# Kernel optimization log

Hardware: AMD Instinct MI355X
Metric: run time of the kernel (lower is better)

## Reference

```python
import jax, jax.numpy as jnp
import numpy as np

N_NODES = 100000
N_EDGES = 320000
DIM = 256


def _graph_conv(src, dst, h, W, b):
    # DGL GraphConv, norm='both', in_feats == out_feats (aggregate-then-transform)
    ones = jnp.ones((src.shape[0],), dtype=h.dtype)
    out_deg = jnp.clip(jax.ops.segment_sum(ones, src, num_segments=N_NODES), 1.0)
    in_deg = jnp.clip(jax.ops.segment_sum(ones, dst, num_segments=N_NODES), 1.0)
    h = h * (out_deg ** -0.5)[:, None]          # src-side normalization
    agg = jax.ops.segment_sum(h[src], dst, num_segments=N_NODES)  # SpMM (copy_u, sum)
    agg = agg * (in_deg ** -0.5)[:, None]       # dst-side normalization
    return agg @ W + b


def setup_inputs() -> dict:
    key = jax.random.key(0)
    ks = jax.random.split(key, 7)
    src = jax.random.randint(ks[0], (N_EDGES,), 0, N_NODES, dtype=jnp.int32)
    dst = jax.random.randint(ks[1], (N_EDGES,), 0, N_NODES, dtype=jnp.int32)
    node_feature = jax.random.normal(ks[2], (N_NODES, DIM), dtype=jnp.float32)
    s = 1.0 / np.sqrt(DIM)
    W1 = jax.random.normal(ks[3], (DIM, DIM), dtype=jnp.float32) * s
    b1 = jnp.zeros((DIM,), dtype=jnp.float32)
    W2 = jax.random.normal(ks[4], (DIM, DIM), dtype=jnp.float32) * s
    b2 = jnp.zeros((DIM,), dtype=jnp.float32)
    return {"src": src, "dst": dst, "node_feature": node_feature,
            "W1": W1, "b1": b1, "W2": W2, "b2": b2}


def reference(src, dst, node_feature, W1, b1, W2, b2):
    h = _graph_conv(src, dst, node_feature, W1, b1)
    h = _graph_conv(src, dst, jax.nn.relu(h), W2, b2)
    return jax.nn.relu(h)
```

## Files before the change

kernel.cpp:

```cpp
#include <hip/hip_runtime.h>

#define NN 100000
#define NE 320000
#define DIM 256
#define ELLW 32
#define FEAT_BLKS (NN * DIM / 4 / 256)

typedef _Float16 half8 __attribute__((ext_vector_type(8)));
typedef _Float16 half4v __attribute__((ext_vector_type(4)));
typedef float float4v __attribute__((ext_vector_type(4)));

__global__ void k_build(const int* __restrict__ src, const int* __restrict__ dst,
                        int* __restrict__ cnt_out, int* __restrict__ cnt_in,
                        int* __restrict__ ell) {
    int e = blockIdx.x * 256 + threadIdx.x;
    if (e < NE) {
        int s = src[e], d = dst[e];
        atomicAdd(&cnt_out[s], 1);
        int slot = atomicAdd(&cnt_in[d], 1);
        if (slot < ELLW) ell[d * ELLW + slot] = s;
    }
}

__global__ __launch_bounds__(256)
void k_prep(const float* __restrict__ feat, const int* __restrict__ cnt_out,
            _Float16* __restrict__ fh,
            const float* __restrict__ W1, const float* __restrict__ W2,
            _Float16* __restrict__ WT1, _Float16* __restrict__ WT2) {
    int b = blockIdx.x;
    if (b < FEAT_BLKS) {
        int i = b * 256 + threadIdx.x;
        int row = i >> 6;
        float w = rsqrtf(fmaxf((float)cnt_out[row], 1.f));
        float4 v = reinterpret_cast<const float4*>(feat)[i];
        half4v o;
        o[0] = (_Float16)(v.x * w); o[1] = (_Float16)(v.y * w);
        o[2] = (_Float16)(v.z * w); o[3] = (_Float16)(v.w * w);
        reinterpret_cast<half4v*>(fh)[i] = o;
    } else {
        int i = (b - FEAT_BLKS) * 256 + threadIdx.x;
        int k = i >> 8, n = i & 255;
        WT1[(size_t)n * DIM + k] = (_Float16)W1[(size_t)k * DIM + n];
        WT2[(size_t)n * DIM + k] = (_Float16)W2[(size_t)k * DIM + n];
    }
}

#define LDA 264

template <typename OutT, bool PRESCALE>
__global__ __launch_bounds__(256)
void k_fused(const int* __restrict__ deg, const int* __restrict__ ell,
             const _Float16* __restrict__ T,
             const _Float16* __restrict__ WT,
             const float* __restrict__ bias,
             const int* __restrict__ cnt_in, const int* __restrict__ cnt_out,
             OutT* __restrict__ out) {
    __shared__ _Float16 As[64 * LDA];

    const int t    = threadIdx.x;
    const int lane = t & 63;
    const int w    = t >> 6;
    const int half = lane >> 5, sl = lane & 31;
    const int bm   = blockIdx.x * 64;
    const int c    = sl << 3;

    int dgv = (lane < 16) ? deg[bm + w * 16 + lane] : 0;

    for (int i = 0; i < 16; ++i) {
        const int r = w * 16 + i;
        const int d = bm + r;
        float acc[8] = {};
        if (d < NN) {
            const size_t e0 = (size_t)d * ELLW;
            const int dg  = __shfl(dgv, i);
            const int cap = min(dg, ELLW);
            int myidx = (lane < 16) ? ell[e0 + lane] : 0;

#define GATHER_ROUND(E0)                                                      \
    {                                                                         \
        bool pa = (E0) + half < cap, pb = (E0) + 2 + half < cap;              \
        int  sa = __shfl(myidx, (E0) + half);                                 \
        int  sb = __shfl(myidx, (E0) + 2 + half);                             \
        half8 va = {}, vb = {};                                               \
        if (pa) va = *reinterpret_cast<const half8*>(T + (size_t)sa * DIM + c); \
        if (pb) vb = *reinterpret_cast<const half8*>(T + (size_t)sb * DIM + c); \
        _Pragma("unroll")                                                     \
        for (int q = 0; q < 8; ++q) acc[q] += (float)va[q] + (float)vb[q];    \
    }
            if (cap > 0)  GATHER_ROUND(0)
            if (cap > 4)  GATHER_ROUND(4)
            if (cap > 8)  GATHER_ROUND(8)
            if (cap > 12) GATHER_ROUND(12)
#undef GATHER_ROUND
            for (int e = 16 + half; e < cap; e += 2) {
                int s = ell[e0 + e];
                half8 v = *reinterpret_cast<const half8*>(T + (size_t)s * DIM + c);
                #pragma unroll
                for (int q = 0; q < 8; ++q) acc[q] += (float)v[q];
            }
        }
        #pragma unroll
        for (int q = 0; q < 8; ++q) acc[q] += __shfl_xor(acc[q], 32);
        if (half == 0) {
            half8 o;
            #pragma unroll
            for (int q = 0; q < 8; ++q) o[q] = (_Float16)acc[q];
            *reinterpret_cast<half8*>(&As[r * LDA + c]) = o;
        }
    }
    __syncthreads();

    const int l15 = lane & 15, quad = lane >> 4;
    const _Float16* bp[4];
    #pragma unroll
    for (int nt = 0; nt < 4; ++nt)
        bp[nt] = WT + (size_t)(w * 64 + nt * 16 + l15) * DIM + quad * 8;

    float4v acc4[4][4] = {};
    for (int k0 = 0; k0 < DIM; k0 += 32) {
        half8 bf[4];
        #pragma unroll
        for (int nt = 0; nt < 4; ++nt)
            bf[nt] = *reinterpret_cast<const half8*>(bp[nt] + k0);
        half8 af[4];
        #pragma unroll
        for (int mt = 0; mt < 4; ++mt)
            af[mt] = *reinterpret_cast<half8*>(&As[(mt * 16 + l15) * LDA + quad * 8 + k0]);
        #pragma unroll
        for (int mt = 0; mt < 4; ++mt)
            #pragma unroll
            for (int nt = 0; nt < 4; ++nt)
                acc4[mt][nt] = __builtin_amdgcn_mfma_f32_16x16x32_f16(af[mt], bf[nt], acc4[mt][nt], 0, 0, 0);
    }

    const int colb = w * 64;
    float bcol[4];
    #pragma unroll
    for (int nt = 0; nt < 4; ++nt)
        bcol[nt] = bias[colb + nt * 16 + l15];

    #pragma unroll
    for (int mt = 0; mt < 4; ++mt) {
        #pragma unroll
        for (int r = 0; r < 4; ++r) {
            int row = bm + mt * 16 + quad * 4 + r;
            if (row < NN) {
                float s  = rsqrtf(fmaxf((float)cnt_in[row], 1.f));
                float ps = PRESCALE ? rsqrtf(fmaxf((float)cnt_out[row], 1.f)) : 1.0f;
                #pragma unroll
                for (int nt = 0; nt < 4; ++nt) {
                    int col = colb + nt * 16 + l15;
                    float v = fmaxf(acc4[mt][nt][r] * s + bcol[nt], 0.f) * ps;
                    out[(size_t)row * DIM + col] = (OutT)v;
                }
            }
        }
    }
}

extern "C" void kernel_launch(void* const* d_in, const int* in_sizes, int n_in,
                              void* d_out, int out_size, void* d_ws, size_t ws_size,
                              hipStream_t stream) {
    const int*   src  = (const int*)d_in[0];
    const int*   dst  = (const int*)d_in[1];
    const float* feat = (const float*)d_in[2];
    const float* W1   = (const float*)d_in[3];
    const float* b1   = (const float*)d_in[4];
    const float* W2   = (const float*)d_in[5];
    const float* b2   = (const float*)d_in[6];
    float* out = (float*)d_out;

    int*      cnt_out = (int*)d_ws;
    int*      cnt_in  = cnt_out + NN;
    int*      ell     = cnt_in + NN;
    _Float16* WT1     = (_Float16*)(ell + (size_t)NN * ELLW);
    _Float16* WT2     = WT1 + DIM * DIM;
    _Float16* fh      = WT2 + DIM * DIM;
    _Float16* h1      = fh + (size_t)NN * DIM;

    hipMemsetAsync(d_ws, 0, (size_t)2 * NN * sizeof(int), stream);

    k_build<<<(NE + 255) / 256, 256, 0, stream>>>(src, dst, cnt_out, cnt_in, ell);
    k_prep <<<FEAT_BLKS + 256, 256, 0, stream>>>(feat, cnt_out, fh, W1, W2, WT1, WT2);

    const int ggrid = (NN + 63) / 64;

    k_fused<_Float16, true ><<<ggrid, 256, 0, stream>>>(cnt_in, ell, fh, WT1, b1, cnt_in, cnt_out, h1);
    k_fused<float,    false><<<ggrid, 256, 0, stream>>>(cnt_in, ell, h1, WT2, b2, cnt_in, cnt_out, out);
}
```

Measured before the change: 414.5 us.

## Use 512-thread blocks with software-pipelined gather and prefetched ELL indices

Each block now uses 8 wavefronts, each aggregating 8 rows instead of 16, so twice as many waves are in flight per tile. Within a wave the gather is double-buffered: the first 8 neighbor loads for the next row are issued before the current row is reduced, and ELL indices for all 8 rows are prefetched up front. The MFMA stage splits output columns into 32 per wave, which halves the accumulator register count. This aims to hide gather memory latency, at the cost of more registers held by the buffered loads and smaller per-wave GEMM tiles.

Result: faster. 365.1 us (-11.9%).

```diff
diff --git a/kernel.cpp b/kernel.cpp
--- a/kernel.cpp
+++ b/kernel.cpp
@@ -48,7 +48,7 @@
 #define LDA 264
 
 template <typename OutT, bool PRESCALE>
-__global__ __launch_bounds__(256)
+__global__ __launch_bounds__(512)
 void k_fused(const int* __restrict__ deg, const int* __restrict__ ell,
              const _Float16* __restrict__ T,
              const _Float16* __restrict__ WT,
@@ -63,81 +63,114 @@
     const int half = lane >> 5, sl = lane & 31;
     const int bm   = blockIdx.x * 64;
     const int c    = sl << 3;
-
-    int dgv = (lane < 16) ? deg[bm + w * 16 + lane] : 0;
-
-    for (int i = 0; i < 16; ++i) {
-        const int r = w * 16 + i;
-        const int d = bm + r;
-        float acc[8] = {};
-        if (d < NN) {
-            const size_t e0 = (size_t)d * ELLW;
-            const int dg  = __shfl(dgv, i);
-            const int cap = min(dg, ELLW);
-            int myidx = (lane < 16) ? ell[e0 + lane] : 0;
-
-#define GATHER_ROUND(E0)                                                      \
-    {                                                                         \
-        bool pa = (E0) + half < cap, pb = (E0) + 2 + half < cap;              \
-        int  sa = __shfl(myidx, (E0) + half);                                 \
-        int  sb = __shfl(myidx, (E0) + 2 + half);                             \
-        half8 va = {}, vb = {};                                               \
-        if (pa) va = *reinterpret_cast<const half8*>(T + (size_t)sa * DIM + c); \
-        if (pb) vb = *reinterpret_cast<const half8*>(T + (size_t)sb * DIM + c); \
-        _Pragma("unroll")                                                     \
-        for (int q = 0; q < 8; ++q) acc[q] += (float)va[q] + (float)vb[q];    \
-    }
-            if (cap > 0)  GATHER_ROUND(0)
-            if (cap > 4)  GATHER_ROUND(4)
-            if (cap > 8)  GATHER_ROUND(8)
-            if (cap > 12) GATHER_ROUND(12)
-#undef GATHER_ROUND
-            for (int e = 16 + half; e < cap; e += 2) {
-                int s = ell[e0 + e];
-                half8 v = *reinterpret_cast<const half8*>(T + (size_t)s * DIM + c);
-                #pragma unroll
-                for (int q = 0; q < 8; ++q) acc[q] += (float)v[q];
-            }
-        }
-        #pragma unroll
-        for (int q = 0; q < 8; ++q) acc[q] += __shfl_xor(acc[q], 32);
-        if (half == 0) {
-            half8 o;
-            #pragma unroll
-            for (int q = 0; q < 8; ++q) o[q] = (_Float16)acc[q];
-            *reinterpret_cast<half8*>(&As[r * LDA + c]) = o;
-        }
-    }
+    const int n0   = bm + w * 8;
+
+    int dgv  = deg[min(n0 + (lane & 7), NN - 1)];
+    int pre0 = ell[(size_t)min(n0 +     (lane >> 4), NN - 1) * ELLW + (lane & 15)];
+    int pre1 = ell[(size_t)min(n0 + 4 + (lane >> 4), NN - 1) * ELLW + (lane & 15)];
+
+    const half8 hz = {};
+
+#define ISSUE(i, va0, vb0, va1, vb1, capv)                                     \
+    {                                                                          \
+        capv = 0;                                                              \
+        va0 = hz; vb0 = hz; va1 = hz; vb1 = hz;                                \
+        if (n0 + (i) < NN) capv = min(__shfl(dgv, (i)), ELLW);                 \
+        int pr  = ((i) < 4) ? pre0 : pre1;                                     \
+        int bse = ((i) & 3) * 16;                                              \
+        int sa0 = __shfl(pr, bse + 0 + half);                                  \
+        int sb0 = __shfl(pr, bse + 2 + half);                                  \
+        int sa1 = __shfl(pr, bse + 4 + half);                                  \
+        int sb1 = __shfl(pr, bse + 6 + half);                                  \
+        if (0 + half < capv) va0 = *reinterpret_cast<const half8*>(T + (size_t)sa0 * DIM + c); \
+        if (2 + half < capv) vb0 = *reinterpret_cast<const half8*>(T + (size_t)sb0 * DIM + c); \
+        if (4 + half < capv) va1 = *reinterpret_cast<const half8*>(T + (size_t)sa1 * DIM + c); \
+        if (6 + half < capv) vb1 = *reinterpret_cast<const half8*>(T + (size_t)sb1 * DIM + c); \
+    }
+
+#define CONSUME(i, va0, vb0, va1, vb1, capv)                                   \
+    {                                                                          \
+        float acc[8];                                                          \
+        _Pragma("unroll")                                                      \
+        for (int q = 0; q < 8; ++q)                                            \
+            acc[q] = ((float)va0[q] + (float)vb0[q]) + ((float)va1[q] + (float)vb1[q]); \
+        if (capv > 8) {             \
+            int pr  = ((i) < 4) ? pre0 : pre1;                                 \
+            int bse = ((i) & 3) * 16;                                          \
+            _Pragma("unroll")                                                  \
+            for (int e0 = 8; e0 < 16; e0 += 4) {                               \
+                bool pa = e0 + half < capv, pb = e0 + 2 + half < capv;         \
+                int  sa = __shfl(pr, bse + e0 + half);                         \
+                int  sb = __shfl(pr, bse + e0 + 2 + half);                     \
+                half8 xa = hz, xb = hz;                                        \
+                if (pa) xa = *reinterpret_cast<const half8*>(T + (size_t)sa * DIM + c); \
+                if (pb) xb = *reinterpret_cast<const half8*>(T + (size_t)sb * DIM + c); \
+                _Pragma("unroll")                                              \
+                for (int q = 0; q < 8; ++q) acc[q] += (float)xa[q] + (float)xb[q]; \
+            }                                                                  \
+            for (int e = 16 + half; e < capv; e += 2) {        \
+                int sg = ell[(size_t)(n0 + (i)) * ELLW + e];                   \
+                half8 xv = *reinterpret_cast<const half8*>(T + (size_t)sg * DIM + c); \
+                _Pragma("unroll")                                              \
+                for (int q = 0; q < 8; ++q) acc[q] += (float)xv[q];            \
+            }                                                                  \
+        }                                                                      \
+        _Pragma("unroll")                                                      \
+        for (int q = 0; q < 8; ++q) acc[q] += __shfl_xor(acc[q], 32);          \
+        if (half == 0) {                                                       \
+            half8 o;                                                           \
+            _Pragma("unroll")                                                  \
+            for (int q = 0; q < 8; ++q) o[q] = (_Float16)acc[q];               \
+            *reinterpret_cast<half8*>(&As[(w * 8 + (i)) * LDA + c]) = o;       \
+        }                                                                      \
+    }
+
+    half8 a0A, b0A, a1A, b1A, a0B, b0B, a1B, b1B;
+    int capA, capB;
+    ISSUE(0, a0A, b0A, a1A, b1A, capA)
+    ISSUE(1, a0B, b0B, a1B, b1B, capB)
+    CONSUME(0, a0A, b0A, a1A, b1A, capA)
+    ISSUE(2, a0A, b0A, a1A, b1A, capA)
+    CONSUME(1, a0B, b0B, a1B, b1B, capB)
+    ISSUE(3, a0B, b0B, a1B, b1B, capB)
+    CONSUME(2, a0A, b0A, a1A, b1A, capA)
+    ISSUE(4, a0A, b0A, a1A, b1A, capA)
+    CONSUME(3, a0B, b0B, a1B, b1B, capB)
+    ISSUE(5, a0B, b0B, a1B, b1B, capB)
+    CONSUME(4, a0A, b0A, a1A, b1A, capA)
+    ISSUE(6, a0A, b0A, a1A, b1A, capA)
+    CONSUME(5, a0B, b0B, a1B, b1B, capB)
+    ISSUE(7, a0B, b0B, a1B, b1B, capB)
+    CONSUME(6, a0A, b0A, a1A, b1A, capA)
+    CONSUME(7, a0B, b0B, a1B, b1B, capB)
+#undef ISSUE
+#undef CONSUME
+
     __syncthreads();
 
     const int l15 = lane & 15, quad = lane >> 4;
-    const _Float16* bp[4];
+    const int colb = w * 32;
+    const _Float16* bp0 = WT + (size_t)(colb +      l15) * DIM + quad * 8;
+    const _Float16* bp1 = WT + (size_t)(colb + 16 + l15) * DIM + quad * 8;
+
+    float4v acc4[4][2] = {};
     #pragma unroll
-    for (int nt = 0; nt < 4; ++nt)
-        bp[nt] = WT + (size_t)(w * 64 + nt * 16 + l15) * DIM + quad * 8;
-
-    float4v acc4[4][4] = {};
     for (int k0 = 0; k0 < DIM; k0 += 32) {
-        half8 bf[4];
-        #pragma unroll
-        for (int nt = 0; nt < 4; ++nt)
-            bf[nt] = *reinterpret_cast<const half8*>(bp[nt] + k0);
+        half8 bf0 = *reinterpret_cast<const half8*>(bp0 + k0);
+        half8 bf1 = *reinterpret_cast<const half8*>(bp1 + k0);
         half8 af[4];
         #pragma unroll
         for (int mt = 0; mt < 4; ++mt)
             af[mt] = *reinterpret_cast<half8*>(&As[(mt * 16 + l15) * LDA + quad * 8 + k0]);
         #pragma unroll
-        for (int mt = 0; mt < 4; ++mt)
-            #pragma unroll
-            for (int nt = 0; nt < 4; ++nt)
-                acc4[mt][nt] = __builtin_amdgcn_mfma_f32_16x16x32_f16(af[mt], bf[nt], acc4[mt][nt], 0, 0, 0);
-    }
-
-    const int colb = w * 64;
-    float bcol[4];
-    #pragma unroll
-    for (int nt = 0; nt < 4; ++nt)
-        bcol[nt] = bias[colb + nt * 16 + l15];
+        for (int mt = 0; mt < 4; ++mt) {
+            acc4[mt][0] = __builtin_amdgcn_mfma_f32_16x16x32_f16(af[mt], bf0, acc4[mt][0], 0, 0, 0);
+            acc4[mt][1] = __builtin_amdgcn_mfma_f32_16x16x32_f16(af[mt], bf1, acc4[mt][1], 0, 0, 0);
+        }
+    }
+
+    float bc0 = bias[colb + l15];
+    float bc1 = bias[colb + 16 + l15];
 
     #pragma unroll
     for (int mt = 0; mt < 4; ++mt) {
@@ -147,12 +180,10 @@
             if (row < NN) {
                 float s  = rsqrtf(fmaxf((float)cnt_in[row], 1.f));
                 float ps = PRESCALE ? rsqrtf(fmaxf((float)cnt_out[row], 1.f)) : 1.0f;
-                #pragma unroll
-                for (int nt = 0; nt < 4; ++nt) {
-                    int col = colb + nt * 16 + l15;
-                    float v = fmaxf(acc4[mt][nt][r] * s + bcol[nt], 0.f) * ps;
-                    out[(size_t)row * DIM + col] = (OutT)v;
-                }
+                float v0 = fmaxf(acc4[mt][0][r] * s + bc0, 0.f) * ps;
+                float v1 = fmaxf(acc4[mt][1][r] * s + bc1, 0.f) * ps;
+                out[(size_t)row * DIM + colb +      l15] = (OutT)v0;
+                out[(size_t)row * DIM + colb + 16 + l15] = (OutT)v1;
             }
         }
     }
@@ -185,6 +216,6 @@
 
     const int ggrid = (NN + 63) / 64;
 
-    k_fused<_Float16, true ><<<ggrid, 256, 0, stream>>>(cnt_in, ell, fh, WT1, b1, cnt_in, cnt_out, h1);
-    k_fused<float,    false><<<ggrid, 256, 0, stream>>>(cnt_in, ell, h1, WT2, b2, cnt_in, cnt_out, out);
-}
+    k_fused<_Float16, true ><<<ggrid, 512, 0, stream>>>(cnt_in, ell, fh, WT1, b1, cnt_in, cnt_out, h1);
+    k_fused<float,    false><<<ggrid, 512, 0, stream>>>(cnt_in, ell, h1, WT2, b2, cnt_in, cnt_out, out);
+}
```
